# Optimization experiments

Measured on AMD Instinct MI355X. Metric: run time of the kernel, lower is better.

The kernel has to match this reference:

```python
import jax, jax.numpy as jnp
import numpy as np

EPS = 1e-5

def conv3x3(x, w, b):
    # x: [B,C,H,W], w: [O,I,3,3]
    y = jax.lax.conv_general_dilated(x, w, window_strides=(1, 1),
                                     padding=((1, 1), (1, 1)),
                                     dimension_numbers=('NCHW', 'OIHW', 'NCHW'))
    return y + b[None, :, None, None]

def batchnorm(x, gamma, beta):
    # training-mode BN: batch stats over (N,H,W), biased variance
    mean = jnp.mean(x, axis=(0, 2, 3), keepdims=True)
    var = jnp.mean((x - mean) ** 2, axis=(0, 2, 3), keepdims=True)
    xn = (x - mean) * jax.lax.rsqrt(var + EPS)
    return xn * gamma[None, :, None, None] + beta[None, :, None, None]

def setup_inputs() -> dict:
    key = jax.random.key(0)
    ks = jax.random.split(key, 5)
    B, C, H, W = 4, 256, 64, 64
    fan = C * 9
    return {
        'x': jax.random.normal(ks[0], (B, C, H, W), jnp.float32),
        'wv': jax.random.normal(ks[1], (C, C, 3, 3), jnp.float32) / np.sqrt(fan),
        'bv': jax.random.normal(ks[2], (C,), jnp.float32) * 0.01,
        'gv': jnp.ones((C,), jnp.float32),
        'betav': jnp.zeros((C,), jnp.float32),
        'ww': jax.random.normal(ks[3], (C, C, 3, 3), jnp.float32) / np.sqrt(fan),
        'bw': jax.random.normal(ks[4], (C,), jnp.float32) * 0.01,
        'gw': jnp.ones((C,), jnp.float32),
        'betaw': jnp.zeros((C,), jnp.float32),
    }

def reference(x, wv, bv, gv, betav, ww, bw, gw, betaw):
    B, C, H, W = x.shape
    N = H * W
    # value branch: conv3x3 + BN -> [B, N, C]
    value = batchnorm(conv3x3(x, wv, bv), gv, betav).reshape(B, C, N)
    key_ = x.reshape(B, C, N)              # [B, C, N]
    query = key_.transpose(0, 2, 1)        # [B, N, C]
    sim = jnp.einsum('bnc,bcm->bnm', query, key_) * (C ** -0.5)  # [B, N, N]
    sim = jax.nn.softmax(sim, axis=-1)
    context = jnp.einsum('bnm,bcm->bcn', sim, value)             # [B, C, N]
    context = context.reshape(B, C, H, W)
    out = jax.nn.relu(batchnorm(conv3x3(context, ww, bw), gw, betaw))
    return out
```

## Files before the change

### kernel.cpp

```cpp
#include <hip/hip_runtime.h>
#include <cstdint>
#include <cstddef>

typedef __attribute__((ext_vector_type(8))) __bf16 bf16x8;
typedef __attribute__((ext_vector_type(4))) __bf16 bf16x4;
typedef __attribute__((ext_vector_type(4))) float  f32x4;

#define NPIX 4096
#define CHN  256

__device__ __forceinline__ void async_copy16(void* lds, const void* g) {
  __builtin_amdgcn_global_load_lds(
      (const __attribute__((address_space(1))) unsigned int*)g,
      (__attribute__((address_space(3))) unsigned int*)lds, 16, 0, 0);
}

__global__ __launch_bounds__(256) void k_transpose_cast(
    const float* __restrict__ X, __bf16* __restrict__ xT)
{
  __shared__ float tile[64][65];
  const int bid = blockIdx.x;
  const int b  = bid >> 8;
  const int pt = (bid >> 2) & 63;
  const int ct = bid & 3;
  const int tid = threadIdx.x;
  const int tc = tid & 63, tr = tid >> 6;
  const float* Xb = X + ((size_t)b*CHN + ct*64)*NPIX + pt*64;
#pragma unroll
  for (int i=0;i<16;++i) {
    int row = tr + i*4;
    tile[row][tc] = Xb[(size_t)row*NPIX + tc];
  }
  __syncthreads();
  __bf16* Tb = xT + ((size_t)b*NPIX + pt*64)*CHN + ct*64;
#pragma unroll
  for (int i=0;i<16;++i) {
    int prow = tr + i*4;
    Tb[(size_t)prow*CHN + tc] = (__bf16)tile[tc][prow];
  }
}

__global__ __launch_bounds__(256) void k_wcast(
    const float* __restrict__ wv, const float* __restrict__ ww,
    __bf16* __restrict__ wvt, __bf16* __restrict__ wwt)
{
  int idx = blockIdx.x*256 + threadIdx.x;
  int t = idx >> 16;
  int o = (idx >> 8) & 255;
  int i = idx & 255;
  size_t src = ((size_t)o*256 + i)*9 + t;
  wvt[idx] = (__bf16)wv[src];
  wwt[idx] = (__bf16)ww[src];
}

__global__ __launch_bounds__(256, 2) void k_conv_tap(
    const __bf16* __restrict__ W9,
    const __bf16* __restrict__ Bt,
    const __bf16* __restrict__ zb,
    __bf16* __restrict__ Y)
{
  __shared__ __bf16 Alds[2][64*64];
  __shared__ __bf16 Blds[2][128*64];
  const int bid0 = blockIdx.x;
  const int bid = (bid0 & 7)*64 + (bid0 >> 3);
  const int b  = bid >> 7;
  const int mt = (bid >> 5) & 3;
  const int nt = bid & 31;
  const int m0 = mt << 6;
  const int p0 = nt << 7;
  const int tid = threadIdx.x;
  const int w = tid >> 6, l = tid & 63;
  const int l15 = l & 15, lhi = l >> 4;
  const int wr = (w >> 1) << 5;
  const int wc = (w & 1) << 6;

  const __bf16* Btb = Bt + ((size_t)b << 20);
  const f32x4 vzero = {0.f,0.f,0.f,0.f};
  f32x4 acc[2][4];
#pragma unroll
  for (int i=0;i<2;++i)
#pragma unroll
    for (int j=0;j<4;++j) acc[i][j] = vzero;

  auto stage = [&](int buf, int it) {
    const int t = it >> 2, kc = it & 3;
    const int dy = t/3 - 1, dx = t%3 - 1;
    const int dq = dy*64 + dx;
    const int k0 = kc << 6;
#pragma unroll
    for (int i=0;i<2;++i) {
      int inst = w*2 + i;
      int s = inst*64 + l;
      int row = s >> 3, ch = s & 7;
      const __bf16* g = W9 + (size_t)t*65536 + (size_t)(m0+row)*256 + k0
                        + ((ch ^ (row & 7)) << 3);
      async_copy16((char*)(&Alds[buf][0]) + inst*1024, g);
    }
#pragma unroll
    for (int i=0;i<4;++i) {
      int inst = w*4 + i;
      int s = inst*64 + l;
      int pp = s >> 3, ch = s & 7;
      int p = p0 + pp;
      int xx = (p & 63) + dx;
      int yy = (p >> 6) + dy;
      bool ok = ((unsigned)xx < 64u) & ((unsigned)yy < 64u);
      const __bf16* g = ok ? (Btb + (size_t)(p + dq)*256 + k0 + ((ch ^ (pp & 7)) << 3))
                           : zb;
      async_copy16((char*)(&Blds[buf][0]) + inst*1024, g);
    }
  };

  stage(0, 0);
#pragma unroll 1
  for (int it=0; it<36; ++it) {
    const int cur = it & 1;
    if (it < 35) {
      stage(cur^1, it+1);
      asm volatile("s_waitcnt vmcnt(6)" ::: "memory");
    } else {
      asm volatile("s_waitcnt vmcnt(0)" ::: "memory");
    }
    __builtin_amdgcn_s_barrier();
    __builtin_amdgcn_sched_barrier(0);

    const char* Ac = (const char*)(&Alds[cur][0]);
    const char* Bc = (const char*)(&Blds[cur][0]);
#pragma unroll
    for (int kk=0; kk<2; ++kk) {
      const int swz = (((kk<<2)+lhi) ^ (l15 & 7)) << 4;
      bf16x8 af[2], bfr[4];
#pragma unroll
      for (int i=0;i<2;++i)
        af[i] = *(const bf16x8*)(Ac + (size_t)(wr + 16*i + l15)*128 + swz);
#pragma unroll
      for (int j=0;j<4;++j)
        bfr[j] = *(const bf16x8*)(Bc + (size_t)(wc + 16*j + l15)*128 + swz);
#pragma unroll
      for (int i=0;i<2;++i)
#pragma unroll
        for (int j=0;j<4;++j)
          acc[i][j] = __builtin_amdgcn_mfma_f32_16x16x32_bf16(af[i], bfr[j], acc[i][j], 0,0,0);
    }
    __builtin_amdgcn_s_barrier();
  }

  __bf16* Yb = Y + ((size_t)b << 20);
#pragma unroll
  for (int i=0;i<2;++i)
#pragma unroll
    for (int j=0;j<4;++j)
#pragma unroll
      for (int r=0;r<4;++r) {
        int row = m0 + wr + 16*i + lhi*4 + r;
        int col = p0 + wc + 16*j + l15;
        Yb[(size_t)row*NPIX + col] = (__bf16)acc[i][j][r];
      }
}

__global__ __launch_bounds__(256) void k_bn_stats(
    const __bf16* __restrict__ Y, const float* __restrict__ gamma,
    const float* __restrict__ beta, float* __restrict__ scale,
    float* __restrict__ shift)
{
  const int c = blockIdx.x;
  const int tid = threadIdx.x;
  float s = 0.f, s2 = 0.f;
#pragma unroll 1
  for (int b=0;b<4;++b) {
    const __bf16* p = Y + ((size_t)b*CHN + c)*NPIX;
#pragma unroll
    for (int i=0;i<2;++i) {
      bf16x8 v = *(const bf16x8*)(p + (tid + i*256)*8);
#pragma unroll
      for (int j=0;j<8;++j) { float f = (float)v[j]; s += f; s2 += f*f; }
    }
  }
#pragma unroll
  for (int d=1; d<64; d<<=1) { s += __shfl_xor(s, d, 64); s2 += __shfl_xor(s2, d, 64); }
  __shared__ float rs[4], rs2[4];
  if ((tid & 63) == 0) { rs[tid>>6] = s; rs2[tid>>6] = s2; }
  __syncthreads();
  if (tid == 0) {
    float S  = rs[0]+rs[1]+rs[2]+rs[3];
    float S2 = rs2[0]+rs2[1]+rs2[2]+rs2[3];
    const float inv_n = 1.f/16384.f;
    float mean = S*inv_n;
    float var  = S2*inv_n - mean*mean;
    float rstd = rsqrtf(var + 1e-5f);
    float sc = gamma[c]*rstd;
    scale[c] = sc;
    shift[c] = beta[c] - mean*sc;
  }
}

__global__ __launch_bounds__(256) void k_bn_apply_bf16(
    const __bf16* __restrict__ Y, const float* __restrict__ scale,
    const float* __restrict__ shift, __bf16* __restrict__ V)
{
  size_t idx = ((size_t)blockIdx.x*256 + threadIdx.x)*8;
  int c = (int)((idx >> 12) & 255);
  bf16x8 v = *(const bf16x8*)(Y + idx);
  float sc = scale[c], sh = shift[c];
  bf16x8 r;
#pragma unroll
  for (int j=0;j<8;++j) r[j] = (__bf16)((float)v[j]*sc + sh);
  *(bf16x8*)(V + idx) = r;
}

__global__ __launch_bounds__(256) void k_bn_relu(
    const __bf16* __restrict__ Y, const float* __restrict__ scale,
    const float* __restrict__ shift, float* __restrict__ out)
{
  size_t idx = ((size_t)blockIdx.x*256 + threadIdx.x)*8;
  int c = (int)((idx >> 12) & 255);
  bf16x8 v = *(const bf16x8*)(Y + idx);
  float sc = scale[c], sh = shift[c];
  float4 r0, r1;
  r0.x = fmaxf((float)v[0]*sc + sh, 0.f);
  r0.y = fmaxf((float)v[1]*sc + sh, 0.f);
  r0.z = fmaxf((float)v[2]*sc + sh, 0.f);
  r0.w = fmaxf((float)v[3]*sc + sh, 0.f);
  r1.x = fmaxf((float)v[4]*sc + sh, 0.f);
  r1.y = fmaxf((float)v[5]*sc + sh, 0.f);
  r1.z = fmaxf((float)v[6]*sc + sh, 0.f);
  r1.w = fmaxf((float)v[7]*sc + sh, 0.f);
  *(float4*)(out + idx)     = r0;
  *(float4*)(out + idx + 4) = r1;
}

__global__ __launch_bounds__(256) void k_attn(
    const __bf16* __restrict__ xT,
    const __bf16* __restrict__ val,
    __bf16* __restrict__ O)
{
  __shared__ __bf16 Klds[2][64*256];
  __shared__ __bf16 Vlds[2][256*64];
  __shared__ __bf16 Pscr[4][16*72];

  const int bid0 = blockIdx.x;
  const int bid = (bid0 & 7)*32 + (bid0 >> 3);
  const int b  = bid >> 6;
  const int q0 = (bid & 63) << 6;
  const int tid = threadIdx.x;
  const int w = tid >> 6, l = tid & 63;
  const int l15 = l & 15, lhi = l >> 4;

  const __bf16* xTb = xT  + ((size_t)b << 20);
  const __bf16* vb  = val + ((size_t)b << 20);

  bf16x8 aq[8];
  {
    const __bf16* qp = xTb + (size_t)(q0 + w*16 + l15)*256 + lhi*8;
#pragma unroll
    for (int kc=0; kc<8; ++kc) {
      bf16x8 v = *(const bf16x8*)(qp + kc*32);
#pragma unroll
      for (int j=0;j<8;++j) v[j] = (__bf16)((float)v[j] * 0.0625f);
      aq[kc] = v;
    }
  }

  auto stage = [&](int buf, int m0) {
    char* kb = (char*)(&Klds[buf][0]);
    char* vv = (char*)(&Vlds[buf][0]);
#pragma unroll
    for (int i=0;i<8;++i) {
      int inst = w*8 + i;
      int s = inst*64 + l;
      int row = s >> 5, cs = s & 31;
      const __bf16* g = xTb + (size_t)(m0 + row)*256 + ((cs ^ (row & 7)) << 3);
      async_copy16(kb + inst*1024, g);
    }
#pragma unroll
    for (int i=0;i<8;++i) {
      int inst = w*8 + i;
      int s = inst*64 + l;
      int row = s >> 3, cs = s & 7;
      const __bf16* g = vb + (size_t)row*NPIX + m0 + ((cs ^ (row & 7)) << 3);
      async_copy16(vv + inst*1024, g);
    }
  };

  const f32x4 vzero = {0.f,0.f,0.f,0.f};
  float lsum[4] = {0.f,0.f,0.f,0.f};
  f32x4 o[16];
#pragma unroll
  for (int cf=0; cf<16; ++cf) o[cf] = vzero;

  stage(0, 0);

#pragma unroll 1
  for (int mt=0; mt<64; ++mt) {
    const int cur = mt & 1;
    if (mt < 63) {
      stage(cur^1, (mt+1) << 6);
      asm volatile("s_waitcnt vmcnt(16)" ::: "memory");
    } else {
      asm volatile("s_waitcnt vmcnt(0)" ::: "memory");
    }
    __builtin_amdgcn_s_barrier();
    __builtin_amdgcn_sched_barrier(0);

    const __bf16* Kc = &Klds[cur][0];
    const __bf16* Vc = &Vlds[cur][0];
    __bf16* pl = &Pscr[w][0];

    f32x4 s4[4];
#pragma unroll
    for (int mf=0; mf<4; ++mf) {
      f32x4 acc = vzero;
      const int row = l15 + (mf<<4);
      const char* kbase = (const char*)Kc + row*512;
#pragma unroll
      for (int kc=0; kc<8; ++kc) {
        bf16x8 bk = *(const bf16x8*)(kbase + ((((kc<<2)+lhi) ^ (row&7)) << 4));
        acc = __builtin_amdgcn_mfma_f32_16x16x32_bf16(aq[kc], bk, acc, 0,0,0);
      }
      s4[mf] = acc;
    }

#pragma unroll
    for (int r=0;r<4;++r) {
      float ps = 0.f;
#pragma unroll
      for (int mf=0; mf<4; ++mf) {
        float p = __expf(s4[mf][r]);
        __bf16 pbf = (__bf16)p;
        pl[(lhi*4+r)*72 + l15 + (mf<<4)] = pbf;
        ps += (float)pbf;
      }
      lsum[r] += ps;
    }
    bf16x8 pa[2];
#pragma unroll
    for (int kk=0;kk<2;++kk)
      pa[kk] = *(const bf16x8*)(pl + l15*72 + kk*32 + lhi*8);

#pragma unroll
    for (int cf=0; cf<16; ++cf) {
      const int c = l15 + (cf<<4);
      const char* vbase = (const char*)Vc + c*128;
#pragma unroll
      for (int kk=0; kk<2; ++kk) {
        bf16x8 bv = *(const bf16x8*)(vbase + ((((kk<<2)+lhi) ^ (c&7)) << 4));
        o[cf] = __builtin_amdgcn_mfma_f32_16x16x32_bf16(pa[kk], bv, o[cf], 0,0,0);
      }
    }
    __builtin_amdgcn_s_barrier();
  }

#pragma unroll
  for (int r=0;r<4;++r) {
#pragma unroll
    for (int d=1; d<16; d<<=1) lsum[r] += __shfl_xor(lsum[r], d, 64);
  }

  __bf16* Ob = O + ((size_t)b << 20);
  float inv[4];
#pragma unroll
  for (int r=0;r<4;++r) inv[r] = 1.f / lsum[r];
#pragma unroll
  for (int cf=0; cf<16; ++cf)
#pragma unroll
    for (int r=0;r<4;++r) {
      int row = q0 + w*16 + lhi*4 + r;
      Ob[(size_t)row*256 + l15 + (cf<<4)] = (__bf16)(o[cf][r] * inv[r]);
    }
}

extern "C" void kernel_launch(void* const* d_in, const int* in_sizes, int n_in,
                              void* d_out, int out_size, void* d_ws, size_t ws_size,
                              hipStream_t stream)
{
  const float* x     = (const float*)d_in[0];
  const float* wv    = (const float*)d_in[1];
  const float* gv    = (const float*)d_in[3];
  const float* betav = (const float*)d_in[4];
  const float* ww    = (const float*)d_in[5];
  const float* gw    = (const float*)d_in[7];
  const float* betaw = (const float*)d_in[8];
  float* out = (float*)d_out;

  char* ws = (char*)d_ws;
  __bf16* xT     = (__bf16*)(ws);
  __bf16* val    = (__bf16*)(ws + 8388608);
  __bf16* Obuf   = (__bf16*)(ws + 16777216);
  __bf16* ybuf   = (__bf16*)(ws + 25165824);
  __bf16* wvt    = (__bf16*)(ws + 33554432);
  __bf16* wwt    = (__bf16*)(ws + 34734080);
  float* scale_v = (float*)(ws + 35913728);
  float* shift_v = (float*)(ws + 35914752);
  float* scale_w = (float*)(ws + 35915776);
  float* shift_w = (float*)(ws + 35916800);
  __bf16* zbuf   = (__bf16*)(ws + 35917824);
  if (ws_size < 35918848) return;

  hipMemsetAsync(zbuf, 0, 1024, stream);

  k_transpose_cast<<<1024, 256, 0, stream>>>(x, xT);
  k_wcast<<<2304, 256, 0, stream>>>(wv, ww, wvt, wwt);

  k_conv_tap<<<512, 256, 0, stream>>>(wvt, xT, zbuf, ybuf);
  k_bn_stats<<<256, 256, 0, stream>>>(ybuf, gv, betav, scale_v, shift_v);
  k_bn_apply_bf16<<<2048, 256, 0, stream>>>(ybuf, scale_v, shift_v, val);

  k_attn<<<256, 256, 0, stream>>>(xT, val, Obuf);

  k_conv_tap<<<512, 256, 0, stream>>>(wwt, Obuf, zbuf, ybuf);
  k_bn_stats<<<256, 256, 0, stream>>>(ybuf, gw, betaw, scale_w, shift_w);
  k_bn_relu<<<2048, 256, 0, stream>>>(ybuf, scale_w, shift_w, out);
}
```

Measured before the change: 244.1 us.

## Split attention waves into 2x2 query/key-value halves with LDS reduction

Each wave now handles 32 query rows and half of each 64-key tile, so every K and V fragment read from LDS feeds two MFMAs instead of one. This halves LDS fragment traffic per MFMA. The partial outputs and row sums from the two key-value halves are combined through an LDS scratch reduction at the end. The prefetch is restructured to issue after a full vmcnt(0) wait and barrier, which drops the trailing barrier but exposes more load latency. Register use doubles for the output accumulators, and launch bounds pin one block per CU.

```diff
diff --git a/kernel.cpp b/kernel.cpp
--- a/kernel.cpp
+++ b/kernel.cpp
@@ -229,14 +229,12 @@
   *(float4*)(out + idx + 4) = r1;
 }
 
-__global__ __launch_bounds__(256) void k_attn(
+__global__ __launch_bounds__(256, 1) void k_attn(
     const __bf16* __restrict__ xT,
     const __bf16* __restrict__ val,
     __bf16* __restrict__ O)
 {
-  __shared__ __bf16 Klds[2][64*256];
-  __shared__ __bf16 Vlds[2][256*64];
-  __shared__ __bf16 Pscr[4][16*72];
+  __shared__ __align__(16) char smem[149504];
 
   const int bid0 = blockIdx.x;
   const int bid = (bid0 & 7)*32 + (bid0 >> 3);
@@ -245,25 +243,28 @@
   const int tid = threadIdx.x;
   const int w = tid >> 6, l = tid & 63;
   const int l15 = l & 15, lhi = l >> 4;
+  const int qh  = w & 1;
+  const int kvh = w >> 1;
 
   const __bf16* xTb = xT  + ((size_t)b << 20);
   const __bf16* vb  = val + ((size_t)b << 20);
 
-  bf16x8 aq[8];
-  {
-    const __bf16* qp = xTb + (size_t)(q0 + w*16 + l15)*256 + lhi*8;
+  bf16x8 aq[2][8];
+#pragma unroll
+  for (int rg=0; rg<2; ++rg) {
+    const __bf16* qp = xTb + (size_t)(q0 + qh*32 + rg*16 + l15)*256 + lhi*8;
 #pragma unroll
     for (int kc=0; kc<8; ++kc) {
       bf16x8 v = *(const bf16x8*)(qp + kc*32);
 #pragma unroll
       for (int j=0;j<8;++j) v[j] = (__bf16)((float)v[j] * 0.0625f);
-      aq[kc] = v;
+      aq[rg][kc] = v;
     }
   }
 
   auto stage = [&](int buf, int m0) {
-    char* kb = (char*)(&Klds[buf][0]);
-    char* vv = (char*)(&Vlds[buf][0]);
+    char* kb = smem + buf*32768;
+    char* vv = smem + 65536 + buf*32768;
 #pragma unroll
     for (int i=0;i<8;++i) {
       int inst = w*8 + i;
@@ -283,90 +284,123 @@
   };
 
   const f32x4 vzero = {0.f,0.f,0.f,0.f};
-  float lsum[4] = {0.f,0.f,0.f,0.f};
-  f32x4 o[16];
-#pragma unroll
-  for (int cf=0; cf<16; ++cf) o[cf] = vzero;
+  float lsum[2][4];
+#pragma unroll
+  for (int rg=0;rg<2;++rg)
+#pragma unroll
+    for (int r=0;r<4;++r) lsum[rg][r] = 0.f;
+  f32x4 o[2][16];
+#pragma unroll
+  for (int rg=0;rg<2;++rg)
+#pragma unroll
+    for (int cf=0; cf<16; ++cf) o[rg][cf] = vzero;
 
   stage(0, 0);
 
 #pragma unroll 1
   for (int mt=0; mt<64; ++mt) {
     const int cur = mt & 1;
-    if (mt < 63) {
-      stage(cur^1, (mt+1) << 6);
-      asm volatile("s_waitcnt vmcnt(16)" ::: "memory");
-    } else {
-      asm volatile("s_waitcnt vmcnt(0)" ::: "memory");
-    }
+    asm volatile("s_waitcnt vmcnt(0)" ::: "memory");
     __builtin_amdgcn_s_barrier();
     __builtin_amdgcn_sched_barrier(0);
-
-    const __bf16* Kc = &Klds[cur][0];
-    const __bf16* Vc = &Vlds[cur][0];
-    __bf16* pl = &Pscr[w][0];
-
-    f32x4 s4[4];
-#pragma unroll
-    for (int mf=0; mf<4; ++mf) {
-      f32x4 acc = vzero;
-      const int row = l15 + (mf<<4);
-      const char* kbase = (const char*)Kc + row*512;
+    if (mt < 63) stage(cur^1, (mt+1) << 6);
+
+    const char* Kc = smem + cur*32768;
+    const char* Vc = smem + 65536 + cur*32768;
+    __bf16* pl = (__bf16*)(smem + 131072 + w*4608);
+
+    f32x4 s4[2][2];
+#pragma unroll
+    for (int rg=0;rg<2;++rg)
+#pragma unroll
+      for (int mf=0;mf<2;++mf) s4[rg][mf] = vzero;
+#pragma unroll
+    for (int mf=0; mf<2; ++mf) {
+      const int row = kvh*32 + l15 + (mf<<4);
+      const char* kbase = Kc + row*512;
 #pragma unroll
       for (int kc=0; kc<8; ++kc) {
         bf16x8 bk = *(const bf16x8*)(kbase + ((((kc<<2)+lhi) ^ (row&7)) << 4));
-        acc = __builtin_amdgcn_mfma_f32_16x16x32_bf16(aq[kc], bk, acc, 0,0,0);
+        s4[0][mf] = __builtin_amdgcn_mfma_f32_16x16x32_bf16(aq[0][kc], bk, s4[0][mf], 0,0,0);
+        s4[1][mf] = __builtin_amdgcn_mfma_f32_16x16x32_bf16(aq[1][kc], bk, s4[1][mf], 0,0,0);
       }
-      s4[mf] = acc;
-    }
-
-#pragma unroll
-    for (int r=0;r<4;++r) {
-      float ps = 0.f;
-#pragma unroll
-      for (int mf=0; mf<4; ++mf) {
-        float p = __expf(s4[mf][r]);
-        __bf16 pbf = (__bf16)p;
-        pl[(lhi*4+r)*72 + l15 + (mf<<4)] = pbf;
-        ps += (float)pbf;
+    }
+
+#pragma unroll
+    for (int rg=0;rg<2;++rg)
+#pragma unroll
+      for (int r=0;r<4;++r) {
+        float ps = 0.f;
+#pragma unroll
+        for (int mf=0; mf<2; ++mf) {
+          float p = __expf(s4[rg][mf][r]);
+          __bf16 pbf = (__bf16)p;
+          pl[(rg*16 + lhi*4 + r)*36 + l15 + (mf<<4)] = pbf;
+          ps += (float)pbf;
+        }
+        lsum[rg][r] += ps;
       }
-      lsum[r] += ps;
-    }
-    bf16x8 pa[2];
-#pragma unroll
-    for (int kk=0;kk<2;++kk)
-      pa[kk] = *(const bf16x8*)(pl + l15*72 + kk*32 + lhi*8);
+    bf16x8 pa0 = *(const bf16x8*)(pl + (size_t)l15*36 + lhi*8);
+    bf16x8 pa1 = *(const bf16x8*)(pl + (size_t)(16 + l15)*36 + lhi*8);
 
 #pragma unroll
     for (int cf=0; cf<16; ++cf) {
       const int c = l15 + (cf<<4);
-      const char* vbase = (const char*)Vc + c*128;
-#pragma unroll
-      for (int kk=0; kk<2; ++kk) {
-        bf16x8 bv = *(const bf16x8*)(vbase + ((((kk<<2)+lhi) ^ (c&7)) << 4));
-        o[cf] = __builtin_amdgcn_mfma_f32_16x16x32_bf16(pa[kk], bv, o[cf], 0,0,0);
-      }
-    }
-    __builtin_amdgcn_s_barrier();
-  }
-
-#pragma unroll
-  for (int r=0;r<4;++r) {
-#pragma unroll
-    for (int d=1; d<16; d<<=1) lsum[r] += __shfl_xor(lsum[r], d, 64);
-  }
-
-  __bf16* Ob = O + ((size_t)b << 20);
-  float inv[4];
-#pragma unroll
-  for (int r=0;r<4;++r) inv[r] = 1.f / lsum[r];
-#pragma unroll
-  for (int cf=0; cf<16; ++cf)
-#pragma unroll
-    for (int r=0;r<4;++r) {
-      int row = q0 + w*16 + lhi*4 + r;
-      Ob[(size_t)row*256 + l15 + (cf<<4)] = (__bf16)(o[cf][r] * inv[r]);
-    }
+      const char* vbase = Vc + c*128;
+      bf16x8 bv = *(const bf16x8*)(vbase + ((((kvh<<2)+lhi) ^ (c&7)) << 4));
+      o[0][cf] = __builtin_amdgcn_mfma_f32_16x16x32_bf16(pa0, bv, o[0][cf], 0,0,0);
+      o[1][cf] = __builtin_amdgcn_mfma_f32_16x16x32_bf16(pa1, bv, o[1][cf], 0,0,0);
+    }
+  }
+
+#pragma unroll
+  for (int rg=0;rg<2;++rg)
+#pragma unroll
+    for (int r=0;r<4;++r)
+#pragma unroll
+      for (int d=1; d<16; d<<=1) lsum[rg][r] += __shfl_xor(lsum[rg][r], d, 64);
+
+  __builtin_amdgcn_s_barrier();
+  float* oscr = (float*)smem;
+  float* lscr = (float*)(smem + 65536);
+  if (w >= 2) {
+    float* od = oscr + (size_t)(w-2)*8192;
+#pragma unroll
+    for (int rg=0;rg<2;++rg)
+#pragma unroll
+      for (int cf=0;cf<16;++cf)
+#pragma unroll
+        for (int r=0;r<4;++r)
+          od[(rg*16 + lhi*4 + r)*256 + l15 + (cf<<4)] = o[rg][cf][r];
+    if (l15 == 0) {
+#pragma unroll
+      for (int rg=0;rg<2;++rg)
+#pragma unroll
+        for (int r=0;r<4;++r)
+          lscr[(w-2)*32 + rg*16 + lhi*4 + r] = lsum[rg][r];
+    }
+  }
+  asm volatile("s_waitcnt lgkmcnt(0)" ::: "memory");
+  __builtin_amdgcn_s_barrier();
+  if (w < 2) {
+    float* od = oscr + (size_t)w*8192;
+    __bf16* Ob = O + ((size_t)b << 20);
+#pragma unroll
+    for (int rg=0;rg<2;++rg) {
+      float inv[4];
+#pragma unroll
+      for (int r=0;r<4;++r)
+        inv[r] = 1.f / (lsum[rg][r] + lscr[w*32 + rg*16 + lhi*4 + r]);
+#pragma unroll
+      for (int cf=0;cf<16;++cf)
+#pragma unroll
+        for (int r=0;r<4;++r) {
+          float vtot = o[rg][cf][r] + od[(rg*16 + lhi*4 + r)*256 + l15 + (cf<<4)];
+          int row = q0 + w*32 + rg*16 + lhi*4 + r;
+          Ob[(size_t)row*256 + l15 + (cf<<4)] = (__bf16)(vtot * inv[r]);
+        }
+    }
+  }
 }
 
 extern "C" void kernel_launch(void* const* d_in, const int* in_sizes, int n_in,
```

New measurement: 238.9 us. 1.02x faster.
